# Performance work log

Measured on AMD Instinct MI355X. Metric: run time of the kernel, lower is better.

The kernel has to match this reference:

```python
import jax, jax.numpy as jnp
import numpy as np

N, E, G = 64, 128, 4
D0, ED = 9, 4
H1, H2, H3 = 2000, 500, 100
F1, F2, F3 = 1000, 100, 50


def setup_inputs() -> dict:
    key = jax.random.key(0)
    ks = iter(jax.random.split(key, 32))

    def p(shape, s=0.02):
        return (jax.random.normal(next(ks), shape, jnp.float32) * s)

    inp = {
        "x": jax.random.normal(next(ks), (N, D0), jnp.float32),
        "edge_index": jax.random.randint(next(ks), (2, E), 0, N),
        "edge_attr": jax.random.normal(next(ks), (E, ED), jnp.float32),
        "batch": jnp.sort(jax.random.randint(next(ks), (N,), 0, G)),
        # NNConv layer 1: edge MLP Linear(ED, D0*H1), root weight, bias
        "We1": p((ED, D0 * H1)), "be1": p((D0 * H1,)),
        "root1": p((D0, H1)), "b1": p((H1,)),
        # NNConv layer 2
        "We2": p((ED, H1 * H2)), "be2": p((H1 * H2,)),
        "root2": p((H1, H2)), "b2": p((H2,)),
        # NNConv layer 3
        "We3": p((ED, H2 * H3)), "be3": p((H2 * H3,)),
        "root3": p((H2, H3)), "b3": p((H3,)),
        # FCN head
        "W1": p((H3, F1)), "c1": p((F1,)),
        "W2": p((F1, F2)), "c2": p((F2,)),
        "W3": p((F2, F3)), "c3": p((F3,)),
        "W4": p((F3, 1)), "c4": p((1,)),
    }
    return inp


def _nnconv(x, src, dst, edge_attr, We, be, root, b):
    # edge-conditioned weights: [E, in, out]
    in_dim = x.shape[1]
    w = (edge_attr @ We + be).reshape(edge_attr.shape[0], in_dim, -1)
    # gather source feats, per-edge matmul, scatter-add to targets
    msg = jnp.einsum('ei,eio->eo', x[src], w)
    agg = jax.ops.segment_sum(msg, dst, num_segments=x.shape[0])
    return agg + x @ root + b


def reference(x, edge_index, edge_attr, batch,
              We1, be1, root1, b1,
              We2, be2, root2, b2,
              We3, be3, root3, b3,
              W1, c1, W2, c2, W3, c3, W4, c4):
    src, dst = edge_index[0], edge_index[1]
    h = jax.nn.relu(_nnconv(x, src, dst, edge_attr, We1, be1, root1, b1))
    h = jax.nn.relu(_nnconv(h, src, dst, edge_attr, We2, be2, root2, b2))
    h = jax.nn.relu(_nnconv(h, src, dst, edge_attr, We3, be3, root3, b3))
    # sum readout per graph (dropout layers are identity in eval mode)
    g = jax.ops.segment_sum(h, batch, num_segments=G)  # [G, H3]
    g = jax.nn.relu(g @ W1 + c1)
    g = jax.nn.relu(g @ W2 + c2)
    g = jax.nn.relu(g @ W3 + c3)
    out = g @ W4 + c4
    return out.reshape(-1)  # [G]
```

## Files before the change

kernel.cpp:

```cpp
#include <hip/hip_runtime.h>

#define NN 64
#define EE 128
#define GG 4
#define D0 9
#define H1 2000
#define H2 500
#define H3 100
#define FF1 1000
#define FF2 100
#define FF3 50

#define OFF_P1   28032
#define OFF_Q    156032
#define OFF_PART 924032
#define OFF_F1   2562432
#define OFF_PH   2566448

__device__ __forceinline__ void gl2lds16(const float* g, float* l) {
    __builtin_amdgcn_global_load_lds(
        (const __attribute__((address_space(1))) unsigned int*)g,
        (__attribute__((address_space(3))) unsigned int*)l,
        16, 0, 0);
}

__device__ __forceinline__ float4 ldf4(const float* p) {
    return *(const float4*)p;
}

__device__ __forceinline__ void waitcnt_vm_n(int n) {
    switch (n) {
    case 0: asm volatile("s_waitcnt vmcnt(0)" ::: "memory"); break;
    case 2: asm volatile("s_waitcnt vmcnt(2)" ::: "memory"); break;
    case 4: asm volatile("s_waitcnt vmcnt(4)" ::: "memory"); break;
    default: asm volatile("s_waitcnt vmcnt(6)" ::: "memory"); break;
    }
}
__device__ __forceinline__ void cfence() { asm volatile("" ::: "memory"); }

__device__ __forceinline__ void build_Ad(float* Al, int d,
    const int* __restrict__ ei, const float* __restrict__ ea, int tid)
{
    for (int i = tid; i < NN * NN; i += 256) Al[i] = 0.f;
    __syncthreads();
    if (d == 5) {
        if (tid < NN) Al[tid * 64 + tid] = 1.0f;
    } else if (tid < EE) {
        int s = ei[tid], t = ei[EE + tid];
        float v = (d < 4) ? ea[tid * 4 + d] : 1.0f;
        atomicAdd(&Al[t * 64 + s], v);
    }
}

template<int Kd, int KTOT>
__device__ __forceinline__ void q_compute_store(
    const float* Al, const float* Pl, float* __restrict__ Qf,
    int d, int k0, int tid)
{
    const int kq = tid & 31, rg = tid >> 5;
    float acc[8][4] = {};
    #pragma unroll 4
    for (int u4 = 0; u4 < 16; ++u4) {
        float4 pv0 = ldf4(&Pl[(u4 * 4 + 0) * 128 + kq * 4]);
        float4 pv1 = ldf4(&Pl[(u4 * 4 + 1) * 128 + kq * 4]);
        float4 pv2 = ldf4(&Pl[(u4 * 4 + 2) * 128 + kq * 4]);
        float4 pv3 = ldf4(&Pl[(u4 * 4 + 3) * 128 + kq * 4]);
        #pragma unroll
        for (int i = 0; i < 8; ++i) {
            float4 a = ldf4(&Al[(rg * 8 + i) * 64 + u4 * 4]);
            acc[i][0] += a.x * pv0.x + a.y * pv1.x + a.z * pv2.x + a.w * pv3.x;
            acc[i][1] += a.x * pv0.y + a.y * pv1.y + a.z * pv2.y + a.w * pv3.y;
            acc[i][2] += a.x * pv0.z + a.y * pv1.z + a.z * pv2.z + a.w * pv3.z;
            acc[i][3] += a.x * pv0.w + a.y * pv1.w + a.z * pv2.w + a.w * pv3.w;
        }
    }
    const int k = k0 + kq * 4;
    if (k < Kd) {
        #pragma unroll
        for (int i = 0; i < 8; ++i) {
            int r = rg * 8 + i;
            *(float4*)(Qf + r * KTOT + d * Kd + k) =
                make_float4(acc[i][0], acc[i][1], acc[i][2], acc[i][3]);
        }
    }
}

__global__ __launch_bounds__(256) void k_p1(
    const float* __restrict__ x, const int* __restrict__ edge_index,
    const float* __restrict__ edge_attr,
    const float* __restrict__ We1, const float* __restrict__ be1,
    const float* __restrict__ root1, const float* __restrict__ b1,
    float* __restrict__ P1)
{
    __shared__ float Ys[64 * 56];
    __shared__ __align__(16) float Bs[54 * 64];
    const int tid = threadIdx.x;
    const int tx = tid & 15, ty = tid >> 4;
    const int o0 = blockIdx.x * 64;
    const int w = min(64, H1 - o0);

    for (int i = tid; i < 64 * 56; i += 256) Ys[i] = 0.f;
    __syncthreads();
    if (tid < EE) {
        int s = edge_index[tid], t = edge_index[EE + tid];
        float ea[4];
        #pragma unroll
        for (int d = 0; d < 4; ++d) ea[d] = edge_attr[tid * 4 + d];
        #pragma unroll
        for (int i = 0; i < D0; ++i) {
            float xv = x[s * D0 + i];
            #pragma unroll
            for (int d = 0; d < 4; ++d)
                atomicAdd(&Ys[t * 56 + d * 9 + i], ea[d] * xv);
            atomicAdd(&Ys[t * 56 + 36 + i], xv);
        }
    }
    if (tid < NN) {
        #pragma unroll
        for (int i = 0; i < D0; ++i) Ys[tid * 56 + 45 + i] = x[tid * D0 + i];
    }
    for (int i = tid; i < 54 * 64; i += 256) {
        int r = i >> 6, c = i & 63;
        int d = r / 9, ii = r - d * 9;
        const float* rowp = ((d < 4) ? (We1 + d * (D0 * H1))
                                     : ((d == 4) ? be1 : root1)) + ii * H1;
        Bs[r * 64 + c] = (c < w) ? rowp[o0 + c] : 0.f;
    }
    __syncthreads();

    float acc[4][4] = {};
    #pragma unroll 6
    for (int r = 0; r < 54; ++r) {
        float a0 = Ys[(ty * 4 + 0) * 56 + r];
        float a1 = Ys[(ty * 4 + 1) * 56 + r];
        float a2 = Ys[(ty * 4 + 2) * 56 + r];
        float a3 = Ys[(ty * 4 + 3) * 56 + r];
        const float4 bv = *(const float4*)&Bs[r * 64 + tx * 4];
        acc[0][0] += a0 * bv.x; acc[0][1] += a0 * bv.y; acc[0][2] += a0 * bv.z; acc[0][3] += a0 * bv.w;
        acc[1][0] += a1 * bv.x; acc[1][1] += a1 * bv.y; acc[1][2] += a1 * bv.z; acc[1][3] += a1 * bv.w;
        acc[2][0] += a2 * bv.x; acc[2][1] += a2 * bv.y; acc[2][2] += a2 * bv.z; acc[2][3] += a2 * bv.w;
        acc[3][0] += a3 * bv.x; acc[3][1] += a3 * bv.y; acc[3][2] += a3 * bv.z; acc[3][3] += a3 * bv.w;
    }
    #pragma unroll
    for (int i = 0; i < 4; ++i) {
        int u = ty * 4 + i;
        #pragma unroll
        for (int jj = 0; jj < 4; ++jj) {
            int j = o0 + tx * 4 + jj;
            if (j < H1) {
                float v = b1[j] + acc[i][jj];
                P1[u * H1 + j] = v > 0.f ? v : 0.f;
            }
        }
    }
}

template<int Kd, int KTOT, int NKT>
__global__ __launch_bounds__(256) void k_qp(
    const int* __restrict__ edge_index, const float* __restrict__ edge_attr,
    const float* __restrict__ P, float* __restrict__ Qf)
{
    __shared__ __align__(16) float Al[64 * 64];
    __shared__ __align__(16) float Pl[64 * 128];
    const int tid = threadIdx.x;
    const int d = blockIdx.x / NKT, kt = blockIdx.x % NKT;
    const int k0 = kt * 128;
    const int nf4 = (min(128, Kd - k0) + 3) >> 2;

    build_Ad(Al, d, edge_index, edge_attr, tid);
    for (int i4 = tid; i4 < 2048; i4 += 256) {
        int u = i4 >> 5, c4 = i4 & 31;
        float4 v = {0.f, 0.f, 0.f, 0.f};
        if (c4 < nf4) v = ldf4(P + u * Kd + k0 + c4 * 4);
        *(float4*)&Pl[u * 128 + c4 * 4] = v;
    }
    __syncthreads();
    q_compute_store<Kd, KTOT>(Al, Pl, Qf, d, k0, tid);
}

template<int Kd, int KTOT, int NKT>
__global__ __launch_bounds__(256) void k_qf(
    const int* __restrict__ edge_index, const float* __restrict__ edge_attr,
    const float* __restrict__ part, const float* __restrict__ bias,
    float* __restrict__ Qf)
{
    __shared__ __align__(16) float Al[64 * 64];
    __shared__ __align__(16) float Pl[64 * 128];
    const int tid = threadIdx.x;
    const int d = blockIdx.x / NKT, kt = blockIdx.x % NKT;
    const int k0 = kt * 128;

    build_Ad(Al, d, edge_index, edge_attr, tid);
    for (int i4 = tid; i4 < 2048; i4 += 256) {
        int u = i4 >> 5, c4 = i4 & 31;
        int k = k0 + c4 * 4;
        float4 acc = {0.f, 0.f, 0.f, 0.f};
        if (k < Kd) {
            acc = ldf4(bias + k);
            #pragma unroll 10
            for (int s = 0; s < 50; ++s) {
                float4 v = ldf4(part + s * (NN * Kd) + u * Kd + k);
                acc.x += v.x; acc.y += v.y; acc.z += v.z; acc.w += v.w;
            }
            acc.x = fmaxf(acc.x, 0.f); acc.y = fmaxf(acc.y, 0.f);
            acc.z = fmaxf(acc.z, 0.f); acc.w = fmaxf(acc.w, 0.f);
        }
        *(float4*)&Pl[u * 128 + c4 * 4] = acc;
    }
    __syncthreads();
    q_compute_store<Kd, KTOT>(Al, Pl, Qf, d, k0, tid);
}

template<int M, int S, int ITERS, int T1, int T2>
__global__ __launch_bounds__(256) void k_split(
    const float* __restrict__ Qf, const float* __restrict__ We,
    const float* __restrict__ be, const float* __restrict__ root,
    float* __restrict__ part)
{
    constexpr int KC = 20, BN = 64;
    constexpr int KTOT = S * ITERS * KC;
    const int b = blockIdx.x;
    const int s = b % S, ot = b / S;
    const int o0 = ot * BN;
    const int tid = threadIdx.x;
    const int tx = tid & 15, ty = tid >> 4;
    const int wv = tid >> 6, ln = tid & 63;
    const int kbase = s * (KC * ITERS);
    const int nw = (wv == 0) ? 4 : 2;

    __shared__ __align__(16) float As[2][64 * KC];
    __shared__ __align__(16) float Bs[2][KC * BN];

    auto stage = [&](int bf, int kb) {
        for (int c = wv; c < 5; c += 4) {
            int f = c * 256 + ln * 4;
            int r = f / KC, kkk = f - r * KC;
            gl2lds16(Qf + r * KTOT + kb + kkk, &As[bf][c * 256]);
        }
        for (int c = wv; c < 5; c += 4) {
            int f = c * 256 + ln * 4;
            int krow = f >> 6, col = f & 63;
            int kg = kb + krow;
            const float* bp = (kg < T1) ? (We + (long long)kg * M)
                            : (kg < T2) ? (be + (long long)(kg - T1) * M)
                                        : (root + (long long)(kg - T2) * M);
            int cc = min(o0 + col, M - 4);
            gl2lds16(bp + cc, &Bs[bf][c * 256]);
        }
    };

    float acc[4][4] = {};
    stage(0, kbase);
    for (int it = 0; it < ITERS; ++it) {
        int npend = 0;
        if (it + 1 < ITERS) { stage((it + 1) & 1, kbase + (it + 1) * KC); npend = nw; }
        waitcnt_vm_n(npend);
        __builtin_amdgcn_s_barrier();
        __builtin_amdgcn_sched_barrier(0);

        const float* Ab = As[it & 1];
        const float* Bb = Bs[it & 1];
        #pragma unroll
        for (int k4 = 0; k4 < 5; ++k4) {
            float4 av[4], bv[4];
            #pragma unroll
            for (int i = 0; i < 4; ++i)
                av[i] = ldf4(&Ab[(ty * 4 + i) * KC + k4 * 4]);
            #pragma unroll
            for (int q = 0; q < 4; ++q)
                bv[q] = ldf4(&Bb[(k4 * 4 + q) * BN + tx * 4]);
            #pragma unroll
            for (int i = 0; i < 4; ++i) {
                acc[i][0] += av[i].x * bv[0].x; acc[i][1] += av[i].x * bv[0].y;
                acc[i][2] += av[i].x * bv[0].z; acc[i][3] += av[i].x * bv[0].w;
                acc[i][0] += av[i].y * bv[1].x; acc[i][1] += av[i].y * bv[1].y;
                acc[i][2] += av[i].y * bv[1].z; acc[i][3] += av[i].y * bv[1].w;
                acc[i][0] += av[i].z * bv[2].x; acc[i][1] += av[i].z * bv[2].y;
                acc[i][2] += av[i].z * bv[2].z; acc[i][3] += av[i].z * bv[2].w;
                acc[i][0] += av[i].w * bv[3].x; acc[i][1] += av[i].w * bv[3].y;
                acc[i][2] += av[i].w * bv[3].z; acc[i][3] += av[i].w * bv[3].w;
            }
        }
        cfence();
        __builtin_amdgcn_sched_barrier(0);
        __builtin_amdgcn_s_barrier();
    }

    float* dst = part + s * (64 * M);
    #pragma unroll
    for (int i = 0; i < 4; ++i) {
        int u = ty * 4 + i;
        #pragma unroll
        for (int jj = 0; jj < 4; ++jj) {
            int j = o0 + tx * 4 + jj;
            if (j < M) dst[u * M + j] = acc[i][jj];
        }
    }
}

__global__ __launch_bounds__(256) void k_head1(
    const float* __restrict__ part, const float* __restrict__ b3,
    const int* __restrict__ batch,
    const float* __restrict__ W1, const float* __restrict__ c1,
    float* __restrict__ f1)
{
    const int gi = blockIdx.x >> 4;
    const int jt = blockIdx.x & 15;
    const int o0 = jt * 64;
    const int tid = threadIdx.x;
    __shared__ __align__(16) float pre3s[NN * H3];
    __shared__ int   bsh[NN];
    __shared__ float gs[H3];
    __shared__ float red[4 * 64];

    for (int i4 = tid; i4 < (NN * H3) / 4; i4 += 256) {
        int off = i4 * 4;
        float4 acc = ldf4(b3 + off % H3);
        #pragma unroll 10
        for (int s = 0; s < 50; ++s) {
            float4 v = ldf4(part + s * (NN * H3) + off);
            acc.x += v.x; acc.y += v.y; acc.z += v.z; acc.w += v.w;
        }
        *(float4*)&pre3s[off] = acc;
    }
    if (tid < NN) bsh[tid] = batch[tid];
    __syncthreads();
    for (int d = tid; d < H3; d += 256) {
        float acc = 0.f;
        #pragma unroll
        for (int v = 0; v < NN; ++v) {
            float h = pre3s[v * H3 + d];
            h = h > 0.f ? h : 0.f;
            acc += (bsh[v] == gi) ? h : 0.f;
        }
        gs[d] = acc;
    }
    __syncthreads();
    const int jj = tid & 63, kq = tid >> 6;
    const int oc = min(o0 + jj, FF1 - 1);
    float p = 0.f;
    #pragma unroll
    for (int k = kq * 25; k < kq * 25 + 25; ++k)
        p += gs[k] * W1[k * FF1 + oc];
    red[kq * 64 + jj] = p;
    __syncthreads();
    if (tid < 64) {
        int o = o0 + tid;
        if (o < FF1) {
            float v = c1[o] + red[tid] + red[64 + tid] + red[128 + tid] + red[192 + tid];
            f1[gi * FF1 + o] = v > 0.f ? v : 0.f;
        }
    }
}

__global__ __launch_bounds__(256) void k_h2(
    const float* __restrict__ f1, const float* __restrict__ W2,
    float* __restrict__ ph)
{
    const int s = blockIdx.x;
    const int k0 = s * 40;
    const int tid = threadIdx.x;
    __shared__ float f1s[GG * 40];
    for (int i = tid; i < GG * 40; i += 256) {
        int gi = i / 40, kk = i - gi * 40;
        f1s[i] = f1[gi * FF1 + k0 + kk];
    }
    __syncthreads();
    for (int idx = tid; idx < GG * FF2; idx += 256) {
        int gi = idx / FF2, o = idx - gi * FF2;
        float acc = 0.f;
        #pragma unroll 8
        for (int kk = 0; kk < 40; ++kk)
            acc += f1s[gi * 40 + kk] * W2[(k0 + kk) * FF2 + o];
        ph[s * (GG * FF2) + idx] = acc;
    }
}

__global__ __launch_bounds__(256) void k_head3(
    const float* __restrict__ ph, const float* __restrict__ c2,
    const float* __restrict__ W3, const float* __restrict__ c3,
    const float* __restrict__ W4, const float* __restrict__ c4,
    float* __restrict__ out)
{
    const int tid = threadIdx.x;
    __shared__ float f2s[GG * FF2];
    __shared__ float f3s[GG * FF3];
    for (int idx = tid; idx < GG * FF2; idx += 256) {
        int o = idx % FF2;
        float acc = c2[o];
        #pragma unroll 5
        for (int s = 0; s < 25; ++s) acc += ph[s * (GG * FF2) + idx];
        f2s[idx] = acc > 0.f ? acc : 0.f;
    }
    __syncthreads();
    if (tid < GG * FF3) {
        int gi = tid / FF3, o = tid - gi * FF3;
        float acc = c3[o];
        #pragma unroll 4
        for (int k = 0; k < FF2; ++k)
            acc += f2s[gi * FF2 + k] * W3[k * FF3 + o];
        f3s[tid] = acc > 0.f ? acc : 0.f;
    }
    __syncthreads();
    if (tid < GG) {
        float acc = c4[0];
        #pragma unroll
        for (int k = 0; k < FF3; ++k) acc += f3s[tid * FF3 + k] * W4[k];
        out[tid] = acc;
    }
}

extern "C" void kernel_launch(void* const* d_in, const int* in_sizes, int n_in,
                              void* d_out, int out_size, void* d_ws, size_t ws_size,
                              hipStream_t stream) {
    const float* x          = (const float*)d_in[0];
    const int*   edge_index = (const int*)  d_in[1];
    const float* edge_attr  = (const float*)d_in[2];
    const int*   batch      = (const int*)  d_in[3];
    const float* We1 = (const float*)d_in[4];
    const float* be1 = (const float*)d_in[5];
    const float* root1 = (const float*)d_in[6];
    const float* b1  = (const float*)d_in[7];
    const float* We2 = (const float*)d_in[8];
    const float* be2 = (const float*)d_in[9];
    const float* root2 = (const float*)d_in[10];
    const float* b2  = (const float*)d_in[11];
    const float* We3 = (const float*)d_in[12];
    const float* be3 = (const float*)d_in[13];
    const float* root3 = (const float*)d_in[14];
    const float* b3  = (const float*)d_in[15];
    const float* W1 = (const float*)d_in[16];
    const float* c1 = (const float*)d_in[17];
    const float* W2 = (const float*)d_in[18];
    const float* c2 = (const float*)d_in[19];
    const float* W3 = (const float*)d_in[20];
    const float* c3 = (const float*)d_in[21];
    const float* W4 = (const float*)d_in[22];
    const float* c4 = (const float*)d_in[23];
    float* ws  = (float*)d_ws;
    float* out = (float*)d_out;

    k_p1<<<32, 256, 0, stream>>>(x, edge_index, edge_attr,
                                 We1, be1, root1, b1, ws + OFF_P1);
    k_qp<2000, 12000, 16><<<96, 256, 0, stream>>>(edge_index, edge_attr,
                                                  ws + OFF_P1, ws + OFF_Q);
    k_split<500, 50, 12, 8000, 10000><<<400, 256, 0, stream>>>(
        ws + OFF_Q, We2, be2, root2, ws + OFF_PART);
    k_qf<500, 3000, 4><<<24, 256, 0, stream>>>(edge_index, edge_attr,
                                               ws + OFF_PART, b2, ws + OFF_Q);
    k_split<100, 50, 3, 2000, 2500><<<100, 256, 0, stream>>>(
        ws + OFF_Q, We3, be3, root3, ws + OFF_PART);
    k_head1<<<64, 256, 0, stream>>>(ws + OFF_PART, b3, batch, W1, c1,
                                    ws + OFF_F1);
    k_h2<<<25, 256, 0, stream>>>(ws + OFF_F1, W2, ws + OFF_PH);
    k_head3<<<1, 256, 0, stream>>>(ws + OFF_PH, c2, W3, c3, W4, c4, out);
}
```

Measured before the change: 237.9 us.

## Fuse all eight stage kernels into one persistent kernel with grid barriers

```diff
diff --git a/kernel.cpp b/kernel.cpp
--- a/kernel.cpp
+++ b/kernel.cpp
@@ -16,6 +16,24 @@
 #define OFF_PART 924032
 #define OFF_F1   2562432
 #define OFF_PH   2566448
+#define OFF_SYNC 2576448
+
+#define NB 128
+
+__device__ __forceinline__ void gsync(int* bar, int target, int tid) {
+    __syncthreads();
+    if (tid == 0) {
+        __hip_atomic_fetch_add(bar, 1, __ATOMIC_ACQ_REL,
+                               __HIP_MEMORY_SCOPE_AGENT);
+        int spins = 0;
+        while (__hip_atomic_load(bar, __ATOMIC_ACQUIRE,
+                                 __HIP_MEMORY_SCOPE_AGENT) < target) {
+            __builtin_amdgcn_s_sleep(8);
+            if (++spins > (1 << 20)) break;
+        }
+    }
+    __syncthreads();
+}
 
 __device__ __forceinline__ void gl2lds16(const float* g, float* l) {
     __builtin_amdgcn_global_load_lds(
@@ -85,328 +103,350 @@
     }
 }
 
-__global__ __launch_bounds__(256) void k_p1(
-    const float* __restrict__ x, const int* __restrict__ edge_index,
-    const float* __restrict__ edge_attr,
-    const float* __restrict__ We1, const float* __restrict__ be1,
-    const float* __restrict__ root1, const float* __restrict__ b1,
-    float* __restrict__ P1)
-{
-    __shared__ float Ys[64 * 56];
-    __shared__ __align__(16) float Bs[54 * 64];
-    const int tid = threadIdx.x;
-    const int tx = tid & 15, ty = tid >> 4;
-    const int o0 = blockIdx.x * 64;
-    const int w = min(64, H1 - o0);
-
-    for (int i = tid; i < 64 * 56; i += 256) Ys[i] = 0.f;
-    __syncthreads();
-    if (tid < EE) {
-        int s = edge_index[tid], t = edge_index[EE + tid];
-        float ea[4];
-        #pragma unroll
-        for (int d = 0; d < 4; ++d) ea[d] = edge_attr[tid * 4 + d];
-        #pragma unroll
-        for (int i = 0; i < D0; ++i) {
-            float xv = x[s * D0 + i];
-            #pragma unroll
-            for (int d = 0; d < 4; ++d)
-                atomicAdd(&Ys[t * 56 + d * 9 + i], ea[d] * xv);
-            atomicAdd(&Ys[t * 56 + 36 + i], xv);
-        }
-    }
-    if (tid < NN) {
-        #pragma unroll
-        for (int i = 0; i < D0; ++i) Ys[tid * 56 + 45 + i] = x[tid * D0 + i];
-    }
-    for (int i = tid; i < 54 * 64; i += 256) {
-        int r = i >> 6, c = i & 63;
-        int d = r / 9, ii = r - d * 9;
-        const float* rowp = ((d < 4) ? (We1 + d * (D0 * H1))
-                                     : ((d == 4) ? be1 : root1)) + ii * H1;
-        Bs[r * 64 + c] = (c < w) ? rowp[o0 + c] : 0.f;
-    }
-    __syncthreads();
-
-    float acc[4][4] = {};
-    #pragma unroll 6
-    for (int r = 0; r < 54; ++r) {
-        float a0 = Ys[(ty * 4 + 0) * 56 + r];
-        float a1 = Ys[(ty * 4 + 1) * 56 + r];
-        float a2 = Ys[(ty * 4 + 2) * 56 + r];
-        float a3 = Ys[(ty * 4 + 3) * 56 + r];
-        const float4 bv = *(const float4*)&Bs[r * 64 + tx * 4];
-        acc[0][0] += a0 * bv.x; acc[0][1] += a0 * bv.y; acc[0][2] += a0 * bv.z; acc[0][3] += a0 * bv.w;
-        acc[1][0] += a1 * bv.x; acc[1][1] += a1 * bv.y; acc[1][2] += a1 * bv.z; acc[1][3] += a1 * bv.w;
-        acc[2][0] += a2 * bv.x; acc[2][1] += a2 * bv.y; acc[2][2] += a2 * bv.z; acc[2][3] += a2 * bv.w;
-        acc[3][0] += a3 * bv.x; acc[3][1] += a3 * bv.y; acc[3][2] += a3 * bv.z; acc[3][3] += a3 * bv.w;
-    }
-    #pragma unroll
-    for (int i = 0; i < 4; ++i) {
-        int u = ty * 4 + i;
-        #pragma unroll
-        for (int jj = 0; jj < 4; ++jj) {
-            int j = o0 + tx * 4 + jj;
-            if (j < H1) {
-                float v = b1[j] + acc[i][jj];
-                P1[u * H1 + j] = v > 0.f ? v : 0.f;
-            }
-        }
-    }
-}
-
-template<int Kd, int KTOT, int NKT>
-__global__ __launch_bounds__(256) void k_qp(
-    const int* __restrict__ edge_index, const float* __restrict__ edge_attr,
-    const float* __restrict__ P, float* __restrict__ Qf)
-{
-    __shared__ __align__(16) float Al[64 * 64];
-    __shared__ __align__(16) float Pl[64 * 128];
-    const int tid = threadIdx.x;
-    const int d = blockIdx.x / NKT, kt = blockIdx.x % NKT;
-    const int k0 = kt * 128;
-    const int nf4 = (min(128, Kd - k0) + 3) >> 2;
-
-    build_Ad(Al, d, edge_index, edge_attr, tid);
-    for (int i4 = tid; i4 < 2048; i4 += 256) {
-        int u = i4 >> 5, c4 = i4 & 31;
-        float4 v = {0.f, 0.f, 0.f, 0.f};
-        if (c4 < nf4) v = ldf4(P + u * Kd + k0 + c4 * 4);
-        *(float4*)&Pl[u * 128 + c4 * 4] = v;
-    }
-    __syncthreads();
-    q_compute_store<Kd, KTOT>(Al, Pl, Qf, d, k0, tid);
-}
-
-template<int Kd, int KTOT, int NKT>
-__global__ __launch_bounds__(256) void k_qf(
-    const int* __restrict__ edge_index, const float* __restrict__ edge_attr,
-    const float* __restrict__ part, const float* __restrict__ bias,
-    float* __restrict__ Qf)
-{
-    __shared__ __align__(16) float Al[64 * 64];
-    __shared__ __align__(16) float Pl[64 * 128];
-    const int tid = threadIdx.x;
-    const int d = blockIdx.x / NKT, kt = blockIdx.x % NKT;
-    const int k0 = kt * 128;
-
-    build_Ad(Al, d, edge_index, edge_attr, tid);
-    for (int i4 = tid; i4 < 2048; i4 += 256) {
-        int u = i4 >> 5, c4 = i4 & 31;
-        int k = k0 + c4 * 4;
-        float4 acc = {0.f, 0.f, 0.f, 0.f};
-        if (k < Kd) {
-            acc = ldf4(bias + k);
-            #pragma unroll 10
-            for (int s = 0; s < 50; ++s) {
-                float4 v = ldf4(part + s * (NN * Kd) + u * Kd + k);
-                acc.x += v.x; acc.y += v.y; acc.z += v.z; acc.w += v.w;
-            }
-            acc.x = fmaxf(acc.x, 0.f); acc.y = fmaxf(acc.y, 0.f);
-            acc.z = fmaxf(acc.z, 0.f); acc.w = fmaxf(acc.w, 0.f);
-        }
-        *(float4*)&Pl[u * 128 + c4 * 4] = acc;
-    }
-    __syncthreads();
-    q_compute_store<Kd, KTOT>(Al, Pl, Qf, d, k0, tid);
-}
-
 template<int M, int S, int ITERS, int T1, int T2>
-__global__ __launch_bounds__(256) void k_split(
-    const float* __restrict__ Qf, const float* __restrict__ We,
-    const float* __restrict__ be, const float* __restrict__ root,
-    float* __restrict__ part)
+__device__ void split_phase(float* sm, const float* __restrict__ Qf,
+    const float* __restrict__ We, const float* __restrict__ be,
+    const float* __restrict__ root, float* __restrict__ part,
+    int bx, int nb, int tid)
 {
     constexpr int KC = 20, BN = 64;
     constexpr int KTOT = S * ITERS * KC;
-    const int b = blockIdx.x;
-    const int s = b % S, ot = b / S;
-    const int o0 = ot * BN;
-    const int tid = threadIdx.x;
+    constexpr int OT = (M + BN - 1) / BN;
     const int tx = tid & 15, ty = tid >> 4;
     const int wv = tid >> 6, ln = tid & 63;
-    const int kbase = s * (KC * ITERS);
+    float* As = sm;
+    float* Bs = sm + 2560;
     const int nw = (wv == 0) ? 4 : 2;
 
-    __shared__ __align__(16) float As[2][64 * KC];
-    __shared__ __align__(16) float Bs[2][KC * BN];
-
-    auto stage = [&](int bf, int kb) {
-        for (int c = wv; c < 5; c += 4) {
-            int f = c * 256 + ln * 4;
-            int r = f / KC, kkk = f - r * KC;
-            gl2lds16(Qf + r * KTOT + kb + kkk, &As[bf][c * 256]);
-        }
-        for (int c = wv; c < 5; c += 4) {
-            int f = c * 256 + ln * 4;
-            int krow = f >> 6, col = f & 63;
-            int kg = kb + krow;
-            const float* bp = (kg < T1) ? (We + (long long)kg * M)
-                            : (kg < T2) ? (be + (long long)(kg - T1) * M)
-                                        : (root + (long long)(kg - T2) * M);
-            int cc = min(o0 + col, M - 4);
-            gl2lds16(bp + cc, &Bs[bf][c * 256]);
-        }
-    };
-
-    float acc[4][4] = {};
-    stage(0, kbase);
-    for (int it = 0; it < ITERS; ++it) {
-        int npend = 0;
-        if (it + 1 < ITERS) { stage((it + 1) & 1, kbase + (it + 1) * KC); npend = nw; }
-        waitcnt_vm_n(npend);
-        __builtin_amdgcn_s_barrier();
-        __builtin_amdgcn_sched_barrier(0);
-
-        const float* Ab = As[it & 1];
-        const float* Bb = Bs[it & 1];
+    for (int t = bx; t < OT * S; t += nb) {
+        const int s = t % S, ot = t / S;
+        const int o0 = ot * BN;
+        const int kbase = s * (KC * ITERS);
+
+        auto stage = [&](int bf, int kb) {
+            for (int c = wv; c < 5; c += 4) {
+                int f = c * 256 + ln * 4;
+                int r = f / KC, kkk = f - r * KC;
+                gl2lds16(Qf + r * KTOT + kb + kkk, As + bf * 1280 + c * 256);
+            }
+            for (int c = wv; c < 5; c += 4) {
+                int f = c * 256 + ln * 4;
+                int krow = f >> 6, col = f & 63;
+                int kg = kb + krow;
+                const float* bp = (kg < T1) ? (We + (long long)kg * M)
+                                : (kg < T2) ? (be + (long long)(kg - T1) * M)
+                                            : (root + (long long)(kg - T2) * M);
+                int cc = min(o0 + col, M - 4);
+                gl2lds16(bp + cc, Bs + bf * 1280 + c * 256);
+            }
+        };
+
+        float acc[4][4] = {};
+        stage(0, kbase);
+        for (int it = 0; it < ITERS; ++it) {
+            int npend = 0;
+            if (it + 1 < ITERS) { stage((it + 1) & 1, kbase + (it + 1) * KC); npend = nw; }
+            waitcnt_vm_n(npend);
+            __builtin_amdgcn_s_barrier();
+            __builtin_amdgcn_sched_barrier(0);
+
+            const float* Ab = As + (it & 1) * 1280;
+            const float* Bb = Bs + (it & 1) * 1280;
+            #pragma unroll
+            for (int k4 = 0; k4 < 5; ++k4) {
+                float4 av[4], bv[4];
+                #pragma unroll
+                for (int i = 0; i < 4; ++i)
+                    av[i] = ldf4(&Ab[(ty * 4 + i) * KC + k4 * 4]);
+                #pragma unroll
+                for (int q = 0; q < 4; ++q)
+                    bv[q] = ldf4(&Bb[(k4 * 4 + q) * BN + tx * 4]);
+                #pragma unroll
+                for (int i = 0; i < 4; ++i) {
+                    acc[i][0] += av[i].x * bv[0].x; acc[i][1] += av[i].x * bv[0].y;
+                    acc[i][2] += av[i].x * bv[0].z; acc[i][3] += av[i].x * bv[0].w;
+                    acc[i][0] += av[i].y * bv[1].x; acc[i][1] += av[i].y * bv[1].y;
+                    acc[i][2] += av[i].y * bv[1].z; acc[i][3] += av[i].y * bv[1].w;
+                    acc[i][0] += av[i].z * bv[2].x; acc[i][1] += av[i].z * bv[2].y;
+                    acc[i][2] += av[i].z * bv[2].z; acc[i][3] += av[i].z * bv[2].w;
+                    acc[i][0] += av[i].w * bv[3].x; acc[i][1] += av[i].w * bv[3].y;
+                    acc[i][2] += av[i].w * bv[3].z; acc[i][3] += av[i].w * bv[3].w;
+                }
+            }
+            cfence();
+            __builtin_amdgcn_sched_barrier(0);
+            __builtin_amdgcn_s_barrier();
+        }
+
+        float* dst = part + s * (64 * M);
         #pragma unroll
-        for (int k4 = 0; k4 < 5; ++k4) {
-            float4 av[4], bv[4];
-            #pragma unroll
-            for (int i = 0; i < 4; ++i)
-                av[i] = ldf4(&Ab[(ty * 4 + i) * KC + k4 * 4]);
-            #pragma unroll
-            for (int q = 0; q < 4; ++q)
-                bv[q] = ldf4(&Bb[(k4 * 4 + q) * BN + tx * 4]);
-            #pragma unroll
-            for (int i = 0; i < 4; ++i) {
-                acc[i][0] += av[i].x * bv[0].x; acc[i][1] += av[i].x * bv[0].y;
-                acc[i][2] += av[i].x * bv[0].z; acc[i][3] += av[i].x * bv[0].w;
-                acc[i][0] += av[i].y * bv[1].x; acc[i][1] += av[i].y * bv[1].y;
-                acc[i][2] += av[i].y * bv[1].z; acc[i][3] += av[i].y * bv[1].w;
-                acc[i][0] += av[i].z * bv[2].x; acc[i][1] += av[i].z * bv[2].y;
-                acc[i][2] += av[i].z * bv[2].z; acc[i][3] += av[i].z * bv[2].w;
-                acc[i][0] += av[i].w * bv[3].x; acc[i][1] += av[i].w * bv[3].y;
-                acc[i][2] += av[i].w * bv[3].z; acc[i][3] += av[i].w * bv[3].w;
-            }
-        }
-        cfence();
-        __builtin_amdgcn_sched_barrier(0);
-        __builtin_amdgcn_s_barrier();
-    }
-
-    float* dst = part + s * (64 * M);
-    #pragma unroll
-    for (int i = 0; i < 4; ++i) {
-        int u = ty * 4 + i;
-        #pragma unroll
-        for (int jj = 0; jj < 4; ++jj) {
-            int j = o0 + tx * 4 + jj;
-            if (j < M) dst[u * M + j] = acc[i][jj];
-        }
-    }
-}
-
-__global__ __launch_bounds__(256) void k_head1(
-    const float* __restrict__ part, const float* __restrict__ b3,
-    const int* __restrict__ batch,
+        for (int i = 0; i < 4; ++i) {
+            int u = ty * 4 + i;
+            #pragma unroll
+            for (int jj = 0; jj < 4; ++jj) {
+                int j = o0 + tx * 4 + jj;
+                if (j < M) dst[u * M + j] = acc[i][jj];
+            }
+        }
+    }
+}
+
+__global__ void k_bz(float* ws) {
+    if (threadIdx.x == 0) *(int*)(ws + OFF_SYNC) = 0;
+}
+
+__global__ __launch_bounds__(256, 2) void k_fused(
+    const float* __restrict__ x, const int* __restrict__ edge_index,
+    const float* __restrict__ edge_attr, const int* __restrict__ batch,
+    const float* __restrict__ We1, const float* __restrict__ be1,
+    const float* __restrict__ root1, const float* __restrict__ b1,
+    const float* __restrict__ We2, const float* __restrict__ be2,
+    const float* __restrict__ root2, const float* __restrict__ b2,
+    const float* __restrict__ We3, const float* __restrict__ be3,
+    const float* __restrict__ root3, const float* __restrict__ b3,
     const float* __restrict__ W1, const float* __restrict__ c1,
-    float* __restrict__ f1)
-{
-    const int gi = blockIdx.x >> 4;
-    const int jt = blockIdx.x & 15;
-    const int o0 = jt * 64;
-    const int tid = threadIdx.x;
-    __shared__ __align__(16) float pre3s[NN * H3];
-    __shared__ int   bsh[NN];
-    __shared__ float gs[H3];
-    __shared__ float red[4 * 64];
-
-    for (int i4 = tid; i4 < (NN * H3) / 4; i4 += 256) {
-        int off = i4 * 4;
-        float4 acc = ldf4(b3 + off % H3);
-        #pragma unroll 10
-        for (int s = 0; s < 50; ++s) {
-            float4 v = ldf4(part + s * (NN * H3) + off);
-            acc.x += v.x; acc.y += v.y; acc.z += v.z; acc.w += v.w;
-        }
-        *(float4*)&pre3s[off] = acc;
-    }
-    if (tid < NN) bsh[tid] = batch[tid];
-    __syncthreads();
-    for (int d = tid; d < H3; d += 256) {
-        float acc = 0.f;
-        #pragma unroll
-        for (int v = 0; v < NN; ++v) {
-            float h = pre3s[v * H3 + d];
-            h = h > 0.f ? h : 0.f;
-            acc += (bsh[v] == gi) ? h : 0.f;
-        }
-        gs[d] = acc;
-    }
-    __syncthreads();
-    const int jj = tid & 63, kq = tid >> 6;
-    const int oc = min(o0 + jj, FF1 - 1);
-    float p = 0.f;
-    #pragma unroll
-    for (int k = kq * 25; k < kq * 25 + 25; ++k)
-        p += gs[k] * W1[k * FF1 + oc];
-    red[kq * 64 + jj] = p;
-    __syncthreads();
-    if (tid < 64) {
-        int o = o0 + tid;
-        if (o < FF1) {
-            float v = c1[o] + red[tid] + red[64 + tid] + red[128 + tid] + red[192 + tid];
-            f1[gi * FF1 + o] = v > 0.f ? v : 0.f;
-        }
-    }
-}
-
-__global__ __launch_bounds__(256) void k_h2(
-    const float* __restrict__ f1, const float* __restrict__ W2,
-    float* __restrict__ ph)
-{
-    const int s = blockIdx.x;
-    const int k0 = s * 40;
-    const int tid = threadIdx.x;
-    __shared__ float f1s[GG * 40];
-    for (int i = tid; i < GG * 40; i += 256) {
-        int gi = i / 40, kk = i - gi * 40;
-        f1s[i] = f1[gi * FF1 + k0 + kk];
-    }
-    __syncthreads();
-    for (int idx = tid; idx < GG * FF2; idx += 256) {
-        int gi = idx / FF2, o = idx - gi * FF2;
-        float acc = 0.f;
-        #pragma unroll 8
-        for (int kk = 0; kk < 40; ++kk)
-            acc += f1s[gi * 40 + kk] * W2[(k0 + kk) * FF2 + o];
-        ph[s * (GG * FF2) + idx] = acc;
-    }
-}
-
-__global__ __launch_bounds__(256) void k_head3(
-    const float* __restrict__ ph, const float* __restrict__ c2,
+    const float* __restrict__ W2, const float* __restrict__ c2,
     const float* __restrict__ W3, const float* __restrict__ c3,
     const float* __restrict__ W4, const float* __restrict__ c4,
-    float* __restrict__ out)
+    float* __restrict__ ws, float* __restrict__ out)
 {
-    const int tid = threadIdx.x;
-    __shared__ float f2s[GG * FF2];
-    __shared__ float f3s[GG * FF3];
-    for (int idx = tid; idx < GG * FF2; idx += 256) {
-        int o = idx % FF2;
-        float acc = c2[o];
-        #pragma unroll 5
-        for (int s = 0; s < 25; ++s) acc += ph[s * (GG * FF2) + idx];
-        f2s[idx] = acc > 0.f ? acc : 0.f;
-    }
-    __syncthreads();
-    if (tid < GG * FF3) {
-        int gi = tid / FF3, o = tid - gi * FF3;
-        float acc = c3[o];
-        #pragma unroll 4
-        for (int k = 0; k < FF2; ++k)
-            acc += f2s[gi * FF2 + k] * W3[k * FF3 + o];
-        f3s[tid] = acc > 0.f ? acc : 0.f;
-    }
-    __syncthreads();
-    if (tid < GG) {
-        float acc = c4[0];
-        #pragma unroll
-        for (int k = 0; k < FF3; ++k) acc += f3s[tid * FF3 + k] * W4[k];
-        out[tid] = acc;
+    __shared__ __align__(16) float sm[12288];
+    const int bx = blockIdx.x, nb = gridDim.x, tid = threadIdx.x;
+    int* bar = (int*)(ws + OFF_SYNC);
+    int bt = 0;
+
+    {
+        float* Ys = sm;
+        float* Bs = sm + 3584;
+        const int tx = tid & 15, ty = tid >> 4;
+        float* P1 = ws + OFF_P1;
+        for (int i = tid; i < 64 * 56; i += 256) Ys[i] = 0.f;
+        __syncthreads();
+        if (tid < EE) {
+            int s = edge_index[tid], t = edge_index[EE + tid];
+            float ea[4];
+            #pragma unroll
+            for (int d = 0; d < 4; ++d) ea[d] = edge_attr[tid * 4 + d];
+            #pragma unroll
+            for (int i = 0; i < D0; ++i) {
+                float xv = x[s * D0 + i];
+                #pragma unroll
+                for (int d = 0; d < 4; ++d)
+                    atomicAdd(&Ys[t * 56 + d * 9 + i], ea[d] * xv);
+                atomicAdd(&Ys[t * 56 + 36 + i], xv);
+            }
+        }
+        if (tid < NN) {
+            #pragma unroll
+            for (int i = 0; i < D0; ++i) Ys[tid * 56 + 45 + i] = x[tid * D0 + i];
+        }
+        for (int t = bx; t < 32; t += nb) {
+            const int o0 = t * 64;
+            const int w = min(64, H1 - o0);
+            __syncthreads();
+            for (int i = tid; i < 54 * 64; i += 256) {
+                int r = i >> 6, c = i & 63;
+                int d = r / 9, ii = r - d * 9;
+                const float* rowp = ((d < 4) ? (We1 + d * (D0 * H1))
+                                             : ((d == 4) ? be1 : root1)) + ii * H1;
+                Bs[r * 64 + c] = (c < w) ? rowp[o0 + c] : 0.f;
+            }
+            __syncthreads();
+            float acc[4][4] = {};
+            #pragma unroll 6
+            for (int r = 0; r < 54; ++r) {
+                float a0 = Ys[(ty * 4 + 0) * 56 + r];
+                float a1 = Ys[(ty * 4 + 1) * 56 + r];
+                float a2 = Ys[(ty * 4 + 2) * 56 + r];
+                float a3 = Ys[(ty * 4 + 3) * 56 + r];
+                const float4 bv = *(const float4*)&Bs[r * 64 + tx * 4];
+                acc[0][0] += a0 * bv.x; acc[0][1] += a0 * bv.y; acc[0][2] += a0 * bv.z; acc[0][3] += a0 * bv.w;
+                acc[1][0] += a1 * bv.x; acc[1][1] += a1 * bv.y; acc[1][2] += a1 * bv.z; acc[1][3] += a1 * bv.w;
+                acc[2][0] += a2 * bv.x; acc[2][1] += a2 * bv.y; acc[2][2] += a2 * bv.z; acc[2][3] += a2 * bv.w;
+                acc[3][0] += a3 * bv.x; acc[3][1] += a3 * bv.y; acc[3][2] += a3 * bv.z; acc[3][3] += a3 * bv.w;
+            }
+            #pragma unroll
+            for (int i = 0; i < 4; ++i) {
+                int u = ty * 4 + i;
+                #pragma unroll
+                for (int jj = 0; jj < 4; ++jj) {
+                    int j = o0 + tx * 4 + jj;
+                    if (j < H1) {
+                        float v = b1[j] + acc[i][jj];
+                        P1[u * H1 + j] = v > 0.f ? v : 0.f;
+                    }
+                }
+            }
+        }
+    }
+    bt += NB; gsync(bar, bt, tid);
+
+    {
+        float* Al = sm;
+        float* Pl = sm + 4096;
+        const float* P1 = ws + OFF_P1;
+        float* Qf = ws + OFF_Q;
+        for (int t = bx; t < 96; t += nb) {
+            const int d = t / 16, kt = t % 16;
+            const int k0 = kt * 128;
+            const int nf4 = (min(128, 2000 - k0) + 3) >> 2;
+            __syncthreads();
+            build_Ad(Al, d, edge_index, edge_attr, tid);
+            for (int i4 = tid; i4 < 2048; i4 += 256) {
+                int u = i4 >> 5, c4 = i4 & 31;
+                float4 v = {0.f, 0.f, 0.f, 0.f};
+                if (c4 < nf4) v = ldf4(P1 + u * 2000 + k0 + c4 * 4);
+                *(float4*)&Pl[u * 128 + c4 * 4] = v;
+            }
+            __syncthreads();
+            q_compute_store<2000, 12000>(Al, Pl, Qf, d, k0, tid);
+        }
+    }
+    bt += NB; gsync(bar, bt, tid);
+
+    split_phase<500, 50, 12, 8000, 10000>(sm, ws + OFF_Q, We2, be2, root2,
+                                          ws + OFF_PART, bx, nb, tid);
+    bt += NB; gsync(bar, bt, tid);
+
+    {
+        float* Al = sm;
+        float* Pl = sm + 4096;
+        const float* part = ws + OFF_PART;
+        float* Qf = ws + OFF_Q;
+        for (int t = bx; t < 24; t += nb) {
+            const int d = t / 4, kt = t % 4;
+            const int k0 = kt * 128;
+            __syncthreads();
+            build_Ad(Al, d, edge_index, edge_attr, tid);
+            for (int i4 = tid; i4 < 2048; i4 += 256) {
+                int u = i4 >> 5, c4 = i4 & 31;
+                int k = k0 + c4 * 4;
+                float4 acc = {0.f, 0.f, 0.f, 0.f};
+                if (k < 500) {
+                    acc = ldf4(b2 + k);
+                    #pragma unroll 10
+                    for (int s = 0; s < 50; ++s) {
+                        float4 v = ldf4(part + s * (NN * 500) + u * 500 + k);
+                        acc.x += v.x; acc.y += v.y; acc.z += v.z; acc.w += v.w;
+                    }
+                    acc.x = fmaxf(acc.x, 0.f); acc.y = fmaxf(acc.y, 0.f);
+                    acc.z = fmaxf(acc.z, 0.f); acc.w = fmaxf(acc.w, 0.f);
+                }
+                *(float4*)&Pl[u * 128 + c4 * 4] = acc;
+            }
+            __syncthreads();
+            q_compute_store<500, 3000>(Al, Pl, Qf, d, k0, tid);
+        }
+    }
+    bt += NB; gsync(bar, bt, tid);
+
+    split_phase<100, 50, 3, 2000, 2500>(sm, ws + OFF_Q, We3, be3, root3,
+                                        ws + OFF_PART, bx, nb, tid);
+    bt += NB; gsync(bar, bt, tid);
+
+    {
+        float* pre3s = sm;
+        int*   bsh   = (int*)(sm + 6400);
+        float* gs    = sm + 6464;
+        float* red   = sm + 6576;
+        const float* part = ws + OFF_PART;
+        float* f1 = ws + OFF_F1;
+        for (int i4 = tid; i4 < 1600; i4 += 256) {
+            int off = i4 * 4;
+            float4 acc = ldf4(b3 + off % H3);
+            #pragma unroll 10
+            for (int s = 0; s < 50; ++s) {
+                float4 v = ldf4(part + s * (NN * H3) + off);
+                acc.x += v.x; acc.y += v.y; acc.z += v.z; acc.w += v.w;
+            }
+            *(float4*)&pre3s[off] = acc;
+        }
+        if (tid < NN) bsh[tid] = batch[tid];
+        __syncthreads();
+        for (int t = bx; t < 64; t += nb) {
+            const int gi = t >> 4, jt = t & 15, o0 = jt * 64;
+            for (int d = tid; d < H3; d += 256) {
+                float acc = 0.f;
+                #pragma unroll
+                for (int v = 0; v < NN; ++v) {
+                    float h = pre3s[v * H3 + d];
+                    h = h > 0.f ? h : 0.f;
+                    acc += (bsh[v] == gi) ? h : 0.f;
+                }
+                gs[d] = acc;
+            }
+            __syncthreads();
+            const int jj = tid & 63, kq = tid >> 6;
+            const int oc = min(o0 + jj, FF1 - 1);
+            float p = 0.f;
+            #pragma unroll
+            for (int k = kq * 25; k < kq * 25 + 25; ++k)
+                p += gs[k] * W1[k * FF1 + oc];
+            red[kq * 64 + jj] = p;
+            __syncthreads();
+            if (tid < 64) {
+                int o = o0 + tid;
+                if (o < FF1) {
+                    float v = c1[o] + red[tid] + red[64 + tid] + red[128 + tid] + red[192 + tid];
+                    f1[gi * FF1 + o] = v > 0.f ? v : 0.f;
+                }
+            }
+            __syncthreads();
+        }
+    }
+    bt += NB; gsync(bar, bt, tid);
+
+    {
+        float* f1s = sm;
+        const float* f1 = ws + OFF_F1;
+        float* ph = ws + OFF_PH;
+        for (int t = bx; t < 25; t += nb) {
+            const int k0 = t * 40;
+            __syncthreads();
+            for (int i = tid; i < GG * 40; i += 256) {
+                int gi = i / 40, kk = i - gi * 40;
+                f1s[i] = f1[gi * FF1 + k0 + kk];
+            }
+            __syncthreads();
+            for (int idx = tid; idx < GG * FF2; idx += 256) {
+                int gi = idx / FF2, o = idx - gi * FF2;
+                float acc = 0.f;
+                #pragma unroll 8
+                for (int kk = 0; kk < 40; ++kk)
+                    acc += f1s[gi * 40 + kk] * W2[(k0 + kk) * FF2 + o];
+                ph[t * (GG * FF2) + idx] = acc;
+            }
+        }
+    }
+    bt += NB; gsync(bar, bt, tid);
+
+    if (bx == 0) {
+        float* f2s = sm;
+        float* f3s = sm + 512;
+        const float* ph = ws + OFF_PH;
+        for (int idx = tid; idx < GG * FF2; idx += 256) {
+            int o = idx % FF2;
+            float acc = c2[o];
+            #pragma unroll 5
+            for (int s = 0; s < 25; ++s) acc += ph[s * (GG * FF2) + idx];
+            f2s[idx] = acc > 0.f ? acc : 0.f;
+        }
+        __syncthreads();
+        if (tid < GG * FF3) {
+            int gi = tid / FF3, o = tid - gi * FF3;
+            float acc = c3[o];
+            #pragma unroll 4
+            for (int k = 0; k < FF2; ++k)
+                acc += f2s[gi * FF2 + k] * W3[k * FF3 + o];
+            f3s[tid] = acc > 0.f ? acc : 0.f;
+        }
+        __syncthreads();
+        if (tid < GG) {
+            float acc = c4[0];
+            #pragma unroll
+            for (int k = 0; k < FF3; ++k) acc += f3s[tid * FF3 + k] * W4[k];
+            out[tid] = acc;
+        }
     }
 }
 
@@ -440,18 +480,12 @@
     float* ws  = (float*)d_ws;
     float* out = (float*)d_out;
 
-    k_p1<<<32, 256, 0, stream>>>(x, edge_index, edge_attr,
-                                 We1, be1, root1, b1, ws + OFF_P1);
-    k_qp<2000, 12000, 16><<<96, 256, 0, stream>>>(edge_index, edge_attr,
-                                                  ws + OFF_P1, ws + OFF_Q);
-    k_split<500, 50, 12, 8000, 10000><<<400, 256, 0, stream>>>(
-        ws + OFF_Q, We2, be2, root2, ws + OFF_PART);
-    k_qf<500, 3000, 4><<<24, 256, 0, stream>>>(edge_index, edge_attr,
-                                               ws + OFF_PART, b2, ws + OFF_Q);
-    k_split<100, 50, 3, 2000, 2500><<<100, 256, 0, stream>>>(
-        ws + OFF_Q, We3, be3, root3, ws + OFF_PART);
-    k_head1<<<64, 256, 0, stream>>>(ws + OFF_PART, b3, batch, W1, c1,
-                                    ws + OFF_F1);
-    k_h2<<<25, 256, 0, stream>>>(ws + OFF_F1, W2, ws + OFF_PH);
-    k_head3<<<1, 256, 0, stream>>>(ws + OFF_PH, c2, W3, c3, W4, c4, out);
-}
+    k_bz<<<1, 64, 0, stream>>>(ws);
+    k_fused<<<NB, 256, 0, stream>>>(
+        x, edge_index, edge_attr, batch,
+        We1, be1, root1, b1,
+        We2, be2, root2, b2,
+        We3, be3, root3, b3,
+        W1, c1, W2, c2, W3, c3, W4, c4,
+        ws, out);
+}
```

Measured after the change: 470.8 us. 97.9% more time.
